# Performance work log

Measured on AMD Instinct MI355X. Metric: run time of the kernel, lower is better.

The kernel has to match this reference:

```python
import jax, jax.numpy as jnp
import numpy as np
from jax import lax

DIM = 512; HEADS = 8; HD = DIM // HEADS; SM = 16; NS = 3
B = 8; HH = 32; WW = 32; N = HH * WW; HL = DIM // 4


def setup_inputs() -> dict:
    key = jax.random.key(0)
    ks = iter(jax.random.split(key, 64))
    def g(shape, s=0.02):
        return jax.random.normal(next(ks), shape, dtype=jnp.float32) * s
    z = lambda *sh: jnp.zeros(sh, jnp.float32)
    inp = {
        'x': jax.random.normal(next(ks), (B, N, DIM), dtype=jnp.float32),
        'H': HH, 'W': WW,
        'qkv_w': g((NS, 3 * DIM, DIM)),
        'proj_w': g((DIM, DIM)), 'proj_b': z(DIM),
        'pos_sw': g((HEADS, SM, HD, 2)), 'neg_sw': g((HEADS, SM, HD, 2)),
        'spec_mix': jnp.ones((HEADS, SM), jnp.float32),
        'ca_w1': g((DIM // 2, DIM)), 'ca_b1': z(DIM // 2),
        'ca_w2': g((HEADS * 4, DIM // 2)), 'ca_b2': z(HEADS * 4),
        'lstm_wih_f': g((4 * HL, DIM)), 'lstm_whh_f': g((4 * HL, HL)),
        'lstm_bih_f': z(4 * HL), 'lstm_bhh_f': z(4 * HL),
        'lstm_wih_b': g((4 * HL, DIM)), 'lstm_whh_b': g((4 * HL, HL)),
        'lstm_bih_b': z(4 * HL), 'lstm_bhh_b': z(4 * HL),
        'mha_in_w': g((3 * DIM, DIM)), 'mha_in_b': z(3 * DIM),
        'mha_out_w': g((DIM, DIM)), 'mha_out_b': z(DIM),
        'ge_w1': g((DIM // 2, DIM)), 'ge_b1': z(DIM // 2),
        'ge_w2': g((HEADS * 2, DIM // 2)), 'ge_b2': z(HEADS * 2),
        'spw': jnp.ones((NS, HEADS, HD), jnp.float32),
        'dwc_w5': g((HD, 1, 5, 5), 0.05), 'dwc_b5': z(HD),
        'dwc_w7': g((HD, 1, 7, 7), 0.05), 'dwc_b7': z(HD),
        'dwc_w9': g((HD, 1, 9, 9), 0.05), 'dwc_b9': z(HD),
        'mode_w': jnp.ones((3,), jnp.float32) / 3.0,
    }
    return inp


def reference(x, H, W, qkv_w, proj_w, proj_b, pos_sw, neg_sw, spec_mix,
              ca_w1, ca_b1, ca_w2, ca_b2,
              lstm_wih_f, lstm_whh_f, lstm_bih_f, lstm_bhh_f,
              lstm_wih_b, lstm_whh_b, lstm_bih_b, lstm_bhh_b,
              mha_in_w, mha_in_b, mha_out_w, mha_out_b,
              ge_w1, ge_b1, ge_w2, ge_b2, spw,
              dwc_w5, dwc_b5, dwc_w7, dwc_b7, dwc_w9, dwc_b9, mode_w):
    Bn, Nn, C = x.shape
    heads = HEADS; hd = C // heads

    # ---------- DynamicContextEncoder ----------
    def lstm_dir(xs, wih, whh, bih, bhh):
        # xs: (N, B, C); PyTorch gate order i,f,g,o
        gates_x = xs @ wih.T + (bih + bhh)
        hdim = whh.shape[1]
        def step(carry, gx):
            h, c = carry
            gi = gx + h @ whh.T
            i, f, gg, o = jnp.split(gi, 4, axis=-1)
            c = jax.nn.sigmoid(f) * c + jax.nn.sigmoid(i) * jnp.tanh(gg)
            h = jax.nn.sigmoid(o) * jnp.tanh(c)
            return (h, c), h
        z0 = jnp.zeros((xs.shape[1], hdim), xs.dtype)
        _, hs = lax.scan(step, (z0, z0), gates_x)
        return hs

    xs = jnp.swapaxes(x, 0, 1)  # (N, B, C)
    h_f = lstm_dir(xs, lstm_wih_f, lstm_whh_f, lstm_bih_f, lstm_bhh_f)
    h_b = lstm_dir(xs[::-1], lstm_wih_b, lstm_whh_b, lstm_bih_b, lstm_bhh_b)[::-1]
    local_ctx = jnp.concatenate([h_f, h_b], -1).mean(0)  # (B, dim//2)
    local_ctx = jnp.pad(local_ctx, ((0, 0), (0, C - local_ctx.shape[1])))

    nh2 = heads // 2; hd2 = C // nh2
    qkv_c = x @ mha_in_w.T + mha_in_b
    qc, kc, vc = jnp.split(qkv_c, 3, -1)
    sh = lambda t: t.reshape(Bn, Nn, nh2, hd2).transpose(0, 2, 1, 3)
    qc, kc, vc = sh(qc), sh(kc), sh(vc)
    attn = jax.nn.softmax(jnp.einsum('bhnd,bhmd->bhnm', qc, kc) / float(np.sqrt(hd2)), -1)
    ac = jnp.einsum('bhnm,bhmd->bhnd', attn, vc).transpose(0, 2, 1, 3).reshape(Bn, Nn, C)
    ac = ac @ mha_out_w.T + mha_out_b
    combined = x.mean(1) + local_ctx + ac.mean(1)
    coeffs = jax.nn.sigmoid(jax.nn.relu(combined @ ca_w1.T + ca_b1) @ ca_w2.T + ca_b2)
    coeffs = coeffs.reshape(Bn, heads, 4)

    # ---------- GradientInformedMixer coefficients (x_grad is zeros) ----------
    gz = jnp.zeros((Bn, C), x.dtype)
    gmix = jax.nn.softmax((jnp.tanh(gz @ ge_w1.T + ge_b1) @ ge_w2.T + ge_b2).reshape(Bn, heads, 2), -1)

    # ---------- SpectralPolarityMixer ----------
    smix = jax.nn.softmax(spec_mix, -1).mean(-1)[None, :, None, None]  # per-head scalar
    wp = (pos_sw[..., 0] + 1j * pos_sw[..., 1])[:, :SM, :SM]
    wn = (neg_sw[..., 0] + 1j * neg_sw[..., 1])[:, :SM, :SM]

    def spectral(t):
        tf = jnp.fft.rfft2(t)[:, :, :SM, :SM]
        tp = jnp.fft.irfft2(tf * wp[None], s=(Nn, hd))
        tn = jnp.fft.irfft2(tf * wn[None], s=(Nn, hd))
        return tp + tn * smix

    def safe_pow(t, p):  # relu(t)**p with safe grads
        tp = jnp.where(t > 0, t, 1.0)
        return jnp.where(t > 0, tp ** p, 0.0)

    mw = jax.nn.softmax(mode_w, 0)
    def dwc(xi, w, b):
        return lax.conv_general_dilated(xi, w, (1, 1), 'SAME',
                                        feature_group_count=xi.shape[1],
                                        dimension_numbers=('NCHW', 'OIHW', 'NCHW')) + b[None, :, None, None]

    c0, c1, c2, c3 = [coeffs[:, :, i][:, :, None, None] for i in range(4)]
    g0, g1 = gmix[:, :, 0][:, :, None, None], gmix[:, :, 1][:, :, None, None]

    outs = []
    for s in range(NS):
        qkv = (x @ qkv_w[s].T).reshape(Bn, Nn, 3, heads, hd).transpose(2, 0, 3, 1, 4)
        q, k, v = qkv[0], qkv[1], qkv[2]  # (B, heads, N, hd)
        q = spectral(q); k = spectral(k)
        p = (1.0 + jnp.abs(spw[s]))[None, :, None, :]
        q_pos = safe_pow(q, p); q_neg = safe_pow(-q, p)
        k_pos = safe_pow(k, p); k_neg = safe_pow(-k, p)
        kvpp = jnp.einsum('bhnd,bhne->bhde', k_pos, v)
        kvnn = jnp.einsum('bhnd,bhne->bhde', k_neg, v)
        z = (jnp.einsum('bhnd,bhd->bhn', q_pos, k_pos.sum(2))
             + jnp.einsum('bhnd,bhd->bhn', q_neg, k_neg.sum(2)) + 1e-6)[..., None]
        same = (c0 * jnp.einsum('bhnd,bhde->bhne', q_pos, kvpp)
                + c1 * jnp.einsum('bhnd,bhde->bhne', q_neg, kvnn)) / z
        opp = (c2 * jnp.einsum('bhnd,bhde->bhne', q_pos, kvnn)
               + c3 * jnp.einsum('bhnd,bhde->bhne', q_neg, kvpp)) / z
        mixed = g0 * same + g1 * opp
        v_img = v.reshape(Bn * heads, H, W, hd).transpose(0, 3, 1, 2)
        vcv = mw[0] * dwc(v_img, dwc_w5, dwc_b5) + mw[1] * dwc(v_img, dwc_w7, dwc_b7) + mw[2] * dwc(v_img, dwc_w9, dwc_b9)
        vcv = vcv.transpose(0, 2, 3, 1).reshape(Bn, heads, Nn, hd)
        outs.append(mixed + vcv)

    out = jnp.stack(outs).mean(0).transpose(0, 2, 1, 3).reshape(Bn, Nn, C)
    return out @ proj_w.T + proj_b
```

## Files before the change

kernel.cpp:

```cpp
#include <hip/hip_runtime.h>
#include <hip/hip_bf16.h>
#include <math.h>

typedef __bf16 bf16x8 __attribute__((ext_vector_type(8)));
typedef __bf16 bf16x4 __attribute__((ext_vector_type(4)));
typedef float  f32x4  __attribute__((ext_vector_type(4)));

#define MFMA(a,b,c) __builtin_amdgcn_mfma_f32_16x16x32_bf16(a, b, c, 0, 0, 0)
#define LOG2E 1.4426950408889634f

static constexpr size_t OFF_R0    = 0;
static constexpr size_t OFF_GXT   = 12582912;
static constexpr size_t OFF_ACCUM = OFF_GXT;
static constexpr size_t OFF_FINAL = OFF_GXT + 4194304;
static constexpr size_t SOFF      = OFF_GXT + 8388608;
static constexpr size_t OFF_ROWSUM= SOFF;
static constexpr size_t OFF_ACMP  = OFF_ROWSUM;
static constexpr size_t OFF_COLW  = OFF_ROWSUM + 32768;
static constexpr size_t OFF_BM    = OFF_COLW;
static constexpr size_t OFF_ACM   = OFF_COLW + 524288;
static constexpr size_t OFF_XMEAN = OFF_ACM + 4096;
static constexpr size_t OFF_LC    = OFF_XMEAN + 4096;
static constexpr size_t OFF_COEF  = OFF_LC + 2048;
static constexpr size_t OFF_GMIX  = OFF_COEF + 256;
// ... 99 lines not shown
    if (dy>=-3 && dy<=3 && dx>=-3 && dx<=3) v += mw[1]*w7[d*49 + (dy+3)*7 + (dx+3)];
    if (dy>=-2 && dy<=2 && dx>=-2 && dx<=2) v += mw[0]*w5[d*25 + (dy+2)*5 + (dx+2)];
    ws[OFF_CONV9+f] = v;
  }
  if (tid<64) ws[OFF_CBIAS+tid] = mw[0]*b5[tid]+mw[1]*b7[tid]+mw[2]*b9[tid];
  for (int f=tid; f<2048; f+=256){
    int h=f>>8, k1=(f>>4)&15, k2=f&15;
    int src = ((h*16+k1)*64 + k2)*2;
    ws[OFF_WEFF+2*f]   = pos_sw[src]   + 0.0625f*neg_sw[src];
    ws[OFF_WEFF+2*f+1] = pos_sw[src+1] + 0.0625f*neg_sw[src+1];
  }
  for (int f=tid; f<1536; f+=256) ws[OFF_PPOW+f] = 1.0f + fabsf(spw[f]);
  for (int f=tid; f<1024; f+=256){
    int e=f>>4, k2=f&15; int ph=(e*k2)&63;
    float th = (float)ph * (6.283185307179586f/64.0f);
    ws[OFF_W2+2*f]   = cosf(th);
    ws[OFF_W2+2*f+1] = -sinf(th);
  }
  __bf16* w1cs = (__bf16*)(ws + OFF_W1CS);
  for (int f=tid; f<32768; f+=256){
    int r=f>>10, m=f&1023; int k1=r&15; int ph=(k1*m)&1023;
    float th = (float)ph * (6.283185307179586f/1024.0f);
    w1cs[f] = (__bf16)((r<16)?cosf(th):-sinf(th));
  }
  __bf16* w1t = (__bf16*)(ws + OFF_W1T);
  for (int f=tid; f<32768; f+=256){
    int n=f>>5, r=f&31; int k1=r&15; int ph=(k1*n)&1023;
    float th = (float)ph * (6.283185307179586f/1024.0f);
    w1t[f] = (__bf16)((r<16)?cosf(th):sinf(th));
  }
}


__device__ __forceinline__ void d_gemm(const __bf16* __restrict__ A, const __bf16* __restrict__ W,
                                       const float* __restrict__ bias, __bf16* __restrict__ C,
                                       int NB_N, int N, int K, int o, int nwg, int tid, char* smraw){
  __bf16 (*As)[40] = (__bf16(*)[40])smraw;
  __bf16 (*Ws)[40] = (__bf16(*)[40])(smraw + 10240);
  int cpx = nwg >> 3;
  int wg = (o & 7)*cpx + (o >> 3);
  int n0 = (wg % NB_N) * 128, m0 = (wg / NB_N) * 128;
  int l = tid & 63, wid = tid >> 6, lr = l & 15, lg = l >> 4;
  int wr = wid >> 1, wc = wid & 1;
  f32x4 acc[4][4];
  #pragma unroll
  for (int i=0;i<4;++i){ acc[i][0]=fz4(); acc[i][1]=fz4(); acc[i][2]=fz4(); acc[i][3]=fz4(); }
  int srow = tid >> 1, sk = (tid & 1) * 16;
  const __bf16* Ap = A + (size_t)(m0 + srow) * K + sk;
  const __bf16* Wp = W + (size_t)(n0 + srow) * K + sk;
  for (int k0 = 0; k0 < K; k0 += 32){
    bf16x8 a0 = *(const bf16x8*)(Ap), a1 = *(const bf16x8*)(Ap+8);
    bf16x8 w0 = *(const bf16x8*)(Wp), w1 = *(const bf16x8*)(Wp+8);
    Ap += 32; Wp += 32;
    __syncthreads();
    *(bf16x8*)&As[srow][sk]   = a0;  *(bf16x8*)&As[srow][sk+8] = a1;
    *(bf16x8*)&Ws[srow][sk]   = w0;  *(bf16x8*)&Ws[srow][sk+8] = w1;
    __syncthreads();
    bf16x8 aF[4], bF[4];
    #pragma unroll
    for (int mf=0;mf<4;++mf) aF[mf] = *(const bf16x8*)&As[wr*64+mf*16+lr][lg*8];
    #pragma unroll
    for (int nf=0;nf<4;++nf) bF[nf] = *(const bf16x8*)&Ws[wc*64+nf*16+lr][lg*8];
    #pragma unroll
    for (int mf=0;mf<4;++mf)
      #pragma unroll
      for (int nf=0;nf<4;++nf) acc[mf][nf] = MFMA(aF[mf], bF[nf], acc[mf][nf]);
  }
  #pragma unroll
  for (int mf=0;mf<4;++mf)
    #pragma unroll
    for (int nf=0;nf<4;++nf){
      int row = m0 + wr*64 + mf*16 + lg*4;
      int col = n0 + wc*64 + nf*16 + lr;
      float bv = bias ? bias[col] : 0.f;
      #pragma unroll
      for (int r=0;r<4;++r) C[(size_t)(row+r)*N + col] = (__bf16)(acc[mf][nf][r] + bv);
    }
}

template<int PHASE>
__device__ __forceinline__ void d_lstm(const float* __restrict__ whh_f, const float* __restrict__ whh_b,
                                       const __bf16* __restrict__ gates, float* __restrict__ lc,
                                       float* __restrict__ state, int bid, int tid, char* smraw){
  int dir = bid >> 3, b = bid & 7;
  const float* __restrict__ whh = dir ? whh_b : whh_f;
  const __bf16* gx = gates + (size_t)b*1048576;
  int w=tid>>6, l=tid&63, lr=l&15, lg=l>>4;
  bf16x8 wf[4][2][4];
  #pragma unroll
  for (int q=0;q<4;++q)
    #pragma unroll
    for (int t=0;t<2;++t)
      #pragma unroll
      for (int kc=0;kc<4;++kc){
        const float* p = whh + (size_t)(q*128 + w*32 + t*16 + lr)*128 + kc*32 + lg*8;
        bf16x8 v;
        #pragma unroll
        for (int j=0;j<8;++j) v[j]=(__bf16)p[j];
        wf[q][t][kc]=v;
      }
  __bf16 (*hbuf)[132] = (__bf16(*)[132])smraw;
  int tsel = l&1, rsel = (l>>1)&3;
  int hrow = w*32 + tsel*16 + lg*4 + rsel;
  float* st = state + bid*768 + tid*3;
  float cs, hs;
  if (PHASE==0){
    for (int i=tid; i<264; i+=256) ((__bf16*)hbuf)[i] = (__bf16)0.0f;
    cs=0.f; hs=0.f;
  } else {
    cs = st[0]; hs = st[1];
    hbuf[0][hrow] = (__bf16)st[2];
  }
  long t0 = (PHASE==0) ? (dir?1023:0) : (dir?511:512);
  long tstride = dir ? -1024 : 1024;
  long toff = t0*1024 + dir*512 + hrow;
  float g0[4], g1[4], g2[4], g3[4];
  #pragma unroll
  for (int q=0;q<4;++q) g0[q] = (float)gx[toff + q*128];
  toff += tstride;
  #pragma unroll
  for (int q=0;q<4;++q) g1[q] = (float)gx[toff + q*128];
  toff += tstride;
  #pragma unroll
  for (int q=0;q<4;++q) g2[q] = (float)gx[toff + q*128];
  toff += tstride;
  #pragma unroll
  for (int q=0;q<4;++q) g3[q] = (float)gx[toff + q*128];
  toff += tstride;
  __syncthreads();

#define LSTM_STEP(RB, WB, G) { \
    float gq[4]; \
    _Pragma("unroll") for (int q=0;q<4;++q) gq[q]=G[q]; \
    _Pragma("unroll") for (int q=0;q<4;++q) G[q] = (float)gx[toff + q*128]; \
    toff += tstride; \
    if (toff < 0) toff = 0; \
    if (toff > 1048000) toff = 1048000; \
    bf16x8 hf[4]; \
    _Pragma("unroll") for (int kc=0;kc<4;++kc) hf[kc] = *(const bf16x8*)&hbuf[RB][kc*32 + lg*8]; \
    f32x4 acc[4][2]; \
    _Pragma("unroll") for (int q=0;q<4;++q){ acc[q][0]=fz4(); acc[q][1]=fz4(); } \
    _Pragma("unroll") for (int kc=0;kc<4;++kc) \
      _Pragma("unroll") for (int q=0;q<4;++q){ \
        acc[q][0] = MFMA(wf[q][0][kc], hf[kc], acc[q][0]); \
        acc[q][1] = MFMA(wf[q][1][kc], hf[kc], acc[q][1]); } \
    float gv[4]; \
    _Pragma("unroll") for (int q=0;q<4;++q){ \
      f32x4 v0 = acc[q][0], v1 = acc[q][1]; \
      float a01 = (rsel&1) ? v0[1] : v0[0]; \
      float a23 = (rsel&1) ? v0[3] : v0[2]; \
      float av  = (rsel&2) ? a23 : a01; \
      float b01 = (rsel&1) ? v1[1] : v1[0]; \
      float b23 = (rsel&1) ? v1[3] : v1[2]; \
      float bv  = (rsel&2) ? b23 : b01; \
      gv[q] = (tsel ? bv : av) + gq[q]; } \
    float ii=sigm(gv[0]), ff=sigm(gv[1]), gg=tanhx(gv[2]), oo=sigm(gv[3]); \
    cs = ff*cs + ii*gg; \
    float hv = oo*tanhx(cs); \
    hs += hv; \
    if (!(l&8)) hbuf[WB][hrow] = (__bf16)hv; \
    asm volatile("s_waitcnt lgkmcnt(0)" ::: "memory"); \
    __builtin_amdgcn_sched_barrier(0); \
    __builtin_amdgcn_s_barrier(); \
    __builtin_amdgcn_sched_barrier(0); }

  for (int it=0; it<128; ++it){
    LSTM_STEP(0, 1, g0)
    LSTM_STEP(1, 0, g1)
    LSTM_STEP(0, 1, g2)
    LSTM_STEP(1, 0, g3)
  }
#undef LSTM_STEP
  if (PHASE==0){
    st[0]=cs; st[1]=hs; st[2]=(float)hbuf[0][hrow];
  } else {
    if (!(l&8)) lc[b*256 + dir*128 + hrow] = hs*(1.f/1024.f);
  }
}

__device__ __forceinline__ void d_xmean(const float* __restrict__ x, float* __restrict__ xpart,
                                        int f, int tid){
  int sl = f & 15, b = f >> 4;
  #pragma unroll
  for (int cc=0; cc<2; ++cc){
    int c = tid + cc*256;
    float s=0.f;
    for (int n=sl*64; n<sl*64+64; ++n) s += x[((size_t)(b*1024+n))*512 + c];
    xpart[((size_t)(b*16+sl))*512 + c] = s;
  }
}

template<int MODE>
__device__ __forceinline__ void d_mha(const __bf16* __restrict__ qkv, float* __restrict__ rowsum,
                                      float* __restrict__ colw, int f, int tid, char* smraw){
  int rb = f & 3, h2 = (f>>2) & 3, b = f >> 4;
  __bf16 (*Qs)[136] = (__bf16(*)[136])smraw;
  __bf16 (*Ks)[136] = (__bf16(*)[136])(smraw + 69632);
  int l=tid&63, w=tid>>6, lr=l&15, lg=l>>4;
  {
    const float qs = LOG2E / sqrtf(128.0f);
    int row = tid;
    const __bf16* p = qkv + ((size_t)(b*1024 + rb*256 + row))*1536 + h2*128;
    #pragma unroll
    for (int cc=0; cc<128; cc+=8){
      bf16x8 u = *(const bf16x8*)(p+cc);
      bf16x8 v;
      #pragma unroll
      for (int j=0;j<8;++j) v[j]=(__bf16)((float)u[j]*qs);
      *(bf16x8*)&Qs[row][cc] = v;
    }
  }
  float rs[4][4];
  if (MODE==1){
    #pragma unroll
    for (int mf=0;mf<4;++mf){ rs[mf][0]=0.f; rs[mf][1]=0.f; rs[mf][2]=0.f; rs[mf][3]=0.f; }
  } else {
    #pragma unroll
    for (int mf=0;mf<4;++mf)
      #pragma unroll
      for (int r=0;r<4;++r)
        rs[mf][r] = 1.0f / rowsum[((size_t)(b*4+h2))*1024 + rb*256 + w*64 + mf*16 + lg*4 + r];
  }
  for (int mc=0; mc<8; ++mc){
    __syncthreads();
    {
      int row = tid>>1, co = (tid&1)*64;
      const __bf16* p = qkv + ((size_t)(b*1024 + mc*128 + row))*1536 + 512 + h2*128 + co;
      #pragma unroll
      for (int cc=0; cc<64; cc+=8)
        *(bf16x8*)&Ks[row][co+cc] = *(const bf16x8*)(p+cc);
    }
    __syncthreads();
    f32x4 acc[4][8];
    #pragma unroll
    for (int mf=0;mf<4;++mf)
      #pragma unroll
      for (int nf=0;nf<8;++nf) acc[mf][nf]=fz4();
    #pragma unroll
    for (int ks=0;ks<4;++ks){
      bf16x8 aF[4], bFv[8];
      #pragma unroll
      for (int mf=0;mf<4;++mf) aF[mf] = *(const bf16x8*)&Qs[w*64+mf*16+lr][ks*32+lg*8];
      #pragma unroll
      for (int nf=0;nf<8;++nf) bFv[nf] = *(const bf16x8*)&Ks[nf*16+lr][ks*32+lg*8];
      #pragma unroll
      for (int mf=0;mf<4;++mf)
        #pragma unroll
        for (int nf=0;nf<8;++nf) acc[mf][nf] = MFMA(aF[mf], bFv[nf], acc[mf][nf]);
    }
    if (MODE==1){
      #pragma unroll
      for (int mf=0;mf<4;++mf)
        #pragma unroll
        for (int nf=0;nf<8;++nf)
          #pragma unroll
          for (int r=0;r<4;++r) rs[mf][r] += exp2f(acc[mf][nf][r]);
    } else {
      #pragma unroll
      for (int nf=0;nf<8;++nf){
        float cv = 0.f;
// ... 96 lines not shown
      hbl[d*32 + 16 + k1] = (__bf16)(-hi*inv);
    }
  }
  __syncthreads();
  const __bf16* w1t = (const __bf16*)(ws + OFF_W1T);
  bf16x8 bF[4];
  #pragma unroll
  for (int nf=0;nf<4;++nf) bF[nf] = *(const bf16x8*)&hbl[(nf*16+lr)*32 + lg*8];
  for (int pass=0; pass<4; ++pass){
    int rowbase = w*256 + pass*64;
    f32x4 acc[4][4];
    #pragma unroll
    for (int mf=0;mf<4;++mf){ acc[mf][0]=fz4(); acc[mf][1]=fz4(); acc[mf][2]=fz4(); acc[mf][3]=fz4(); }
    #pragma unroll
    for (int mf=0;mf<4;++mf){
      bf16x8 aF = *(const bf16x8*)(w1t + (size_t)(rowbase+mf*16+lr)*32 + lg*8);
      #pragma unroll
      for (int nf=0;nf<4;++nf) acc[mf][nf] = MFMA(aF, bF[nf], acc[mf][nf]);
    }
    #pragma unroll
    for (int mf=0;mf<4;++mf)
      #pragma unroll
      for (int nf=0;nf<4;++nf)
        #pragma unroll
        for (int r=0;r<4;++r){
          int n = rowbase + mf*16 + lg*4 + r;
          int d = nf*16 + lr;
          qkv[((size_t)(b*1024+n))*1536 + colbase + d] = (__bf16)acc[mf][nf][r];
        }
  }
}

__device__ __forceinline__ void d_conv(const __bf16* __restrict__ qkv, const float* __restrict__ ws,
                                       float* __restrict__ accum, int f, int tid, char* smraw, bool init){
  int sl = f & 3, h = (f>>2)&7, b = f>>5;
  float (*vs)[16] = (float(*)[16])smraw;
  float (*wc)[81] = (float(*)[81])(smraw + 65536);
  float* cb       = (float*)(smraw + 65536 + 5184);
  #pragma unroll
  for (int it=0; it<8; ++it){
    int flat = tid + 256*it;
    int pix = flat>>1, cg = (flat&1)*8;
    bf16x8 u = *(const bf16x8*)(qkv + ((size_t)(b*1024+pix))*1536 + 1024 + h*64 + sl*16 + cg);
    #pragma unroll
    for (int j=0;j<8;++j) vs[pix][cg+j] = (float)u[j];
  }
  for (int f2=tid; f2<16*81; f2+=256) wc[f2/81][f2%81] = ws[OFF_CONV9 + (size_t)(sl*16 + f2/81)*81 + (f2%81)];
  if (tid<16) cb[tid] = ws[OFF_CBIAS + sl*16 + tid];
  __syncthreads();
  #pragma unroll
  for (int cc=0; cc<2; ++cc){
    int col = tid + 256*cc;
    int c = col & 15, x = col >> 4;
    float a[32];
    #pragma unroll
    for (int y=0;y<32;++y) a[y]=0.f;
    #pragma unroll
    for (int dx=-4; dx<=4; ++dx){
      int xx = x+dx;
      bool xv = (xx>=0)&&(xx<32);
      float colv[40];
      #pragma unroll
      for (int i=0;i<40;++i){
        int yy = i-4;
        colv[i] = (xv && yy>=0 && yy<32) ? vs[yy*32+xx][c] : 0.f;
      }
      #pragma unroll
      for (int dy=0; dy<9; ++dy){
        float wv = wc[c][dy*9 + dx+4];
        #pragma unroll
        for (int y=0;y<32;++y) a[y] += wv*colv[y+dy];
      }
    }
    float bias = cb[c];
    #pragma unroll
    for (int y=0;y<32;++y){
      size_t oi = ((size_t)((b*8+h)*1024) + y*32 + x)*64 + sl*16 + c;
      if (init) accum[oi] = a[y] + bias;
      else      accum[oi] += a[y] + bias;
    }
  }
}


__global__ __launch_bounds__(256,2) void k_gemm_bf(const __bf16* __restrict__ A, const __bf16* __restrict__ W,
                                                   const float* __restrict__ bias, __bf16* __restrict__ C,
                                                   int NB_N, int N, int K){
  __shared__ __align__(16) char sm[20480];
  d_gemm(A, W, bias, C, NB_N, N, K, blockIdx.x, gridDim.x, threadIdx.x, sm);
}

__global__ __launch_bounds__(256,1) void k_mega1(const float* __restrict__ whh_f, const float* __restrict__ whh_b,
                                                 const __bf16* __restrict__ gates, float* __restrict__ ws,
                                                 const float* __restrict__ x,
                                                 const __bf16* __restrict__ xb, const __bf16* __restrict__ mwb,
                                                 const __bf16* __restrict__ qwb,
                                                 const float* __restrict__ mha_in_b,
                                                 __bf16* __restrict__ qkvA, __bf16* __restrict__ qkvB){
  __shared__ __align__(16) char sm[20480];
  int bid = blockIdx.x, tid = threadIdx.x;
  if (bid < 16)         d_lstm<0>(whh_f, whh_b, gates, ws+OFF_LC, ws+OFF_STATE, bid, tid, sm);
  else if (bid < 784)   d_gemm(xb, mwb, mha_in_b, qkvA, 12, 1536, 512, bid-16, 768, tid, sm);
  else if (bid < 1552)  d_gemm(xb, qwb, nullptr,   qkvB, 12, 1536, 512, bid-784, 768, tid, sm);
  else                  d_xmean(x, ws+OFF_XP2, bid-1552, tid);
}

__global__ __launch_bounds__(256,1) void k_mega2(const float* __restrict__ whh_f, const float* __restrict__ whh_b,
                                                 const __bf16* __restrict__ gates, float* __restrict__ ws,
                                                 const __bf16* __restrict__ qkvA, __bf16* __restrict__ qkvB,
                                                 float* __restrict__ accum){
  __shared__ __align__(16) char sm[104448];
  int bid = blockIdx.x, tid = threadIdx.x;
  if (bid < 16)        d_lstm<1>(whh_f, whh_b, gates, ws+OFF_LC, ws+OFF_STATE, bid, tid, sm);
  else if (bid < 144)  d_spec(qkvB, ws, bid-16, tid, sm);
  else if (bid < 272)  d_mha<1>(qkvA, ws+OFF_ROWSUM, ws+OFF_COLW, bid-144, tid, sm);
  else                 d_conv(qkvB, ws, accum, bid-272, tid, sm, true);
}

__global__ __launch_bounds__(256,2) void k_specconv(__bf16* __restrict__ qkv, const float* __restrict__ ws,
                                                    float* __restrict__ accum){
  __shared__ __align__(16) char sm[80896];
  int bid = blockIdx.x, tid = threadIdx.x;
  if (bid < 128) d_spec(qkv, ws, bid, tid, sm);
  else           d_conv(qkv, ws, accum, bid-128, tid, sm, false);
}

__global__ __launch_bounds__(256,1) void k_mha2_w(const __bf16* __restrict__ qkv, float* __restrict__ rowsum,
                                                  float* __restrict__ colw){
  __shared__ __align__(16) char sm[104448];
  d_mha<2>(qkv, rowsum, colw, blockIdx.x, threadIdx.x, sm);
}

__global__ void k_mha3(const __bf16* __restrict__ qkv, const float* __restrict__ colw, float* __restrict__ acmp){
  int h2 = blockIdx.x, b = blockIdx.y, ms = blockIdx.z;
  int tid = threadIdx.x;
  __shared__ float cwred[128];
  if (tid < 128){
    float cw=0.f;
    #pragma unroll
    for (int t16=0;t16<16;++t16) cw += colw[(((size_t)t16*8 + b)*4 + h2)*1024 + ms*128 + tid];
    cwred[tid]=cw;
  }
  __syncthreads();
  int e = tid & 127, half = tid >> 7;
  float s = 0.f;
  for (int ml = half*64; ml < half*64+64; ++ml)
    s += cwred[ml] * (float)qkv[((size_t)(b*1024 + ms*128 + ml))*1536 + 1024 + h2*128 + e];
  __shared__ float red[256];
  red[tid]=s; __syncthreads();
  if (tid<128) acmp[((size_t)(ms*8+b))*512 + h2*128 + e] = red[tid]+red[tid+128];
}

__global__ __launch_bounds__(256) void k_coeffs(float* __restrict__ ws,
                        const float* __restrict__ mow, const float* __restrict__ mob,
                        const float* __restrict__ ca_w1, const float* __restrict__ ca_b1,
                        const float* __restrict__ ca_w2, const float* __restrict__ ca_b2){
  int b = blockIdx.x, tid = threadIdx.x;
  __shared__ float av[512], comb[512], hid[256];
  for (int i=tid;i<512;i+=256){
    float s = 0.f;
    #pragma unroll
    for (int ms=0; ms<8; ++ms) s += ws[OFF_ACMP + ((size_t)(ms*8+b))*512 + i];
    av[i] = s*(1.f/1024.f);
  }
  __syncthreads();
  for (int c=tid;c<512;c+=256){
    float s = mob[c];
    for (int k=0;k<512;++k) s += mow[(size_t)c*512+k]*av[k];
    float xm = 0.f;
    #pragma unroll
    for (int sl=0; sl<16; ++sl) xm += ws[OFF_XP2 + ((size_t)(b*16+sl))*512 + c];
    comb[c] = s + xm*(1.f/1024.f) + ((c<256) ? ws[OFF_LC + b*256 + c] : 0.f);
  }
  __syncthreads();
  for (int j=tid;j<256;j+=256){
    float s = ca_b1[j];
    for (int k=0;k<512;++k) s += ca_w1[(size_t)j*512+k]*comb[k];
    hid[j] = fmaxf(s,0.f);
  }
  __syncthreads();
  if (tid<32){
    float s = ca_b2[tid];
    for (int k=0;k<256;++k) s += ca_w2[tid*256+k]*hid[k];
    ws[OFF_COEF + b*32 + tid] = 1.f/(1.f+expf(-s));
  }
}

__global__ __launch_bounds__(256,2) void k_polar_kv(const __bf16* __restrict__ qkv, float* __restrict__ ws,
                                                    int s){
  int h = blockIdx.x, b = blockIdx.y;
  int tid=threadIdx.x, l=tid&63, w=tid>>6, lr=l&15, lg=l>>4;
  __shared__ float plds[14300];
  __bf16* kpT = (__bf16*)plds;
  __bf16* knT = (__bf16*)((char*)plds + 17408);
  __bf16* vT  = (__bf16*)((char*)plds + 34816);
  float* scal = (float*)((char*)plds + 56576);
  float* pvs  = scal + 8;
  if (tid<4)  scal[tid] = ws[OFF_COEF + b*32 + h*4 + tid];
  if (tid==4) scal[4] = ws[OFF_GMIX + 2*h];
  if (tid==5) scal[5] = ws[OFF_GMIX + 2*h+1];
  if (tid<64) pvs[tid] = ws[OFF_PPOW + ((size_t)s*8+h)*64 + tid];
  for (int i=tid; i<16*136; i+=256) vT[64*136 + i] = (__bf16)((i<136)?1.0f:0.0f);
  f32x4 acc[4][5];
  #pragma unroll
  for (int mf=0;mf<4;++mf)
    #pragma unroll
    for (int nf=0;nf<5;++nf) acc[mf][nf]=fz4();
  for (int mc=0;mc<8;++mc){
    __syncthreads();
    #pragma unroll
    for (int it=0; it<16; ++it){
      int flat = tid + 256*it;
      int d = flat & 63, np = flat >> 6;
      int n = mc*128 + 2*np;
      const __bf16* kr = qkv + ((size_t)(b*1024+n))*1536 + 512 + h*64 + d;
      const __bf16* vr = qkv + ((size_t)(b*1024+n))*1536 + 1024 + h*64 + d;
      float p = pvs[d];
      float k0=(float)kr[0], k1=(float)kr[1536];
      float kp0,kn0,kp1,kn1;
      powpair(k0,p,kp0,kn0); powpair(k1,p,kp1,kn1);
      *(unsigned*)&kpT[d*136 + 2*np] = pk2(kp0,kp1);
      *(unsigned*)&knT[d*136 + 2*np] = pk2(kn0,kn1);
      *(unsigned*)&vT [d*136 + 2*np] = pk2b(vr[0], vr[1536]);
    }
    __syncthreads();
    const __bf16* A = (w&2)?knT:kpT;
    int kh = (w&1)*64;
    #pragma unroll
    for (int ks=0;ks<2;++ks){
      bf16x8 aF[4];
      #pragma unroll
      for (int mf=0;mf<4;++mf) aF[mf] = *(const bf16x8*)&A[(mf*16+lr)*136 + kh + ks*32 + lg*8];
      #pragma unroll
      for (int nf=0;nf<5;++nf){
        bf16x8 bFv = *(const bf16x8*)&vT[(nf*16+lr)*136 + kh + ks*32 + lg*8];
        #pragma unroll
        for (int mf=0;mf<4;++mf) acc[mf][nf] = MFMA(aF[mf], bFv, acc[mf][nf]);
      }
    }
  }
  __syncthreads();
  float* kvf = plds;
  if ((w&1)==0){
    int mat = w>>1;
    #pragma unroll
    for (int mf=0;mf<4;++mf)
      #pragma unroll
      for (int nf=0;nf<5;++nf)
        #pragma unroll
        for (int r=0;r<4;++r)
          kvf[((size_t)mat*64 + mf*16+lg*4+r)*80 + nf*16+lr] = acc[mf][nf][r];
  }
  __syncthreads();
  if (w&1){
    int mat = w>>1;
    #pragma unroll
    for (int mf=0;mf<4;++mf)
      #pragma unroll
      for (int nf=0;nf<5;++nf)
        #pragma unroll
        for (int r=0;r<4;++r)
          kvf[((size_t)mat*64 + mf*16+lg*4+r)*80 + nf*16+lr] += acc[mf][nf][r];
  }
  __syncthreads();
  __bf16* bmg = (__bf16*)(ws + OFF_BM) + (size_t)(b*8+h)*10240;
  {
    float c0=scal[0], c1=scal[1], c2=scal[2], c3=scal[3], g0=scal[4], g1=scal[5];
    for (int f=tid; f<80*128; f+=256){
      int e=f>>7, kk=f&127;
      float v;
      if (e<64){
        if (kk<64) v = g0*c0*kvf[kk*80+e] + g1*c2*kvf[(64+kk)*80+e];
        else { int k2=kk-64; v = g0*c1*kvf[(64+k2)*80+e] + g1*c3*kvf[k2*80+e]; }
      } else if (e==64){
        v = (kk<64) ? kvf[kk*80+64] : kvf[(64+(kk-64))*80+64];
      } else v = 0.f;
      bmg[f] = (__bf16)v;
    }
  }
}

__global__ __launch_bounds__(256,2) void k_polar_ap(const __bf16* __restrict__ qkv, const float* __restrict__ ws,
                                                    float* __restrict__ accum, int s){
  int pass8 = blockIdx.x, h = blockIdx.y, b = blockIdx.z;
  int tid=threadIdx.x, l=tid&63, w=tid>>6, lr=l&15, lg=l>>4;
  __shared__ __bf16 At[128*136];
  __shared__ __bf16 BmL[80*136];
  __shared__ float zb[128];
  __shared__ float pvs[64];
  if (tid<64) pvs[tid] = ws[OFF_PPOW + ((size_t)s*8+h)*64 + tid];
  {
    const __bf16* bmg = (const __bf16*)(ws + OFF_BM) + (size_t)(b*8+h)*10240;
    for (int u=tid; u<80*16; u+=256){
      int e=u>>4, kx=(u&15)*8;
      *(bf16x8*)&BmL[e*136+kx] = *(const bf16x8*)(bmg + e*128 + kx);
    }
  }
  __syncthreads();
  #pragma unroll
  for (int it=0; it<8; ++it){
    int flat = tid + 256*it;
    int row = flat>>4, dg = flat&15;
    int n = pass8*128 + row;
    const __bf16* qr = qkv + ((size_t)(b*1024+n))*1536 + h*64 + dg*4;
    bf16x4 u = *(const bf16x4*)qr;
    float qp[4], qn[4];
    #pragma unroll
    for (int j=0;j<4;++j) powpair((float)u[j], pvs[dg*4+j], qp[j], qn[j]);
    *(unsigned*)&At[row*136 + dg*4]        = pk2(qp[0],qp[1]);
    *(unsigned*)&At[row*136 + dg*4+2]      = pk2(qp[2],qp[3]);
    *(unsigned*)&At[row*136 + 64 + dg*4]   = pk2(qn[0],qn[1]);
    *(unsigned*)&At[row*136 + 64 + dg*4+2] = pk2(qn[2],qn[3]);
  }
  __syncthreads();
  f32x4 a2[2][5];
  #pragma unroll
  for (int mf=0;mf<2;++mf)
    #pragma unroll
    for (int nf=0;nf<5;++nf) a2[mf][nf]=fz4();
  #pragma unroll
  for (int ks=0;ks<4;++ks){
    bf16x8 aF[2];
    #pragma unroll
    for (int mf=0;mf<2;++mf) aF[mf] = *(const bf16x8*)&At[(w*32+mf*16+lr)*136 + ks*32 + lg*8];
    #pragma unroll
    for (int nf=0;nf<5;++nf){
      bf16x8 bFv = *(const bf16x8*)&BmL[(nf*16+lr)*136 + ks*32 + lg*8];
      #pragma unroll
      for (int mf=0;mf<2;++mf) a2[mf][nf] = MFMA(aF[mf], bFv, a2[mf][nf]);
    }
  }
  if (lr==0){
    #pragma unroll
    for (int mf=0;mf<2;++mf)
      #pragma unroll
      for (int r=0;r<4;++r) zb[w*32 + mf*16 + lg*4 + r] = a2[mf][4][r] + 1e-6f;
  }
  __syncthreads();
  #pragma unroll
  for (int mf=0;mf<2;++mf){
    float rz[4];
    #pragma unroll
    for (int r=0;r<4;++r) rz[r] = 1.0f / zb[w*32 + mf*16 + lg*4 + r];
    #pragma unroll
    for (int nf=0;nf<4;++nf)
      #pragma unroll
      for (int r=0;r<4;++r){
        int n = pass8*128 + w*32 + mf*16 + lg*4 + r;
        int e = nf*16 + lr;
        size_t oi = ((size_t)((b*8+h)*1024) + n)*64 + e;
        accum[oi] += a2[mf][nf][r]*rz[r];
      }
  }
}

__global__ __launch_bounds__(256,2) void k_gemm_acc(const float* __restrict__ accum, const __bf16* __restrict__ W,
                                                    const float* __restrict__ bias, float* __restrict__ C){
  const int N = 512, K = 512, NB_N = 4;
  __shared__ __bf16 As[128][40];
  __shared__ __bf16 Ws[128][40];
  int tid = threadIdx.x;
  int nwg = gridDim.x, o = blockIdx.x;
  int cpx = nwg >> 3;
  int wg = (o & 7)*cpx + (o >> 3);
  int n0 = (wg % NB_N) * 128, m0 = (wg / NB_N) * 128;
  int l = tid & 63, wid = tid >> 6, lr = l & 15, lg = l >> 4;
  int wr = wid >> 1, wc = wid & 1;
  f32x4 acc[4][4];
  #pragma unroll
  for (int i=0;i<4;++i){ acc[i][0]=fz4(); acc[i][1]=fz4(); acc[i][2]=fz4(); acc[i][3]=fz4(); }
  int srow = tid >> 1, sk = (tid & 1) * 16;
  int row = m0 + srow;
  int bb = row >> 10, nn = row & 1023;
  const float* Abase = accum + ((size_t)bb*8192 + nn)*64;
  const __bf16* Wp = W + (size_t)(n0 + srow) * K + sk;
  const float s3 = 1.0f/3.0f;
  for (int k0 = 0; k0 < K; k0 += 32){
    int c0 = k0 + sk;
    const float* Ap = Abase + (size_t)(c0>>6)*65536 + (c0&63);
    f32x4 a0=*(const f32x4*)(Ap), a1=*(const f32x4*)(Ap+4), a2=*(const f32x4*)(Ap+8), a3=*(const f32x4*)(Ap+12);
    bf16x8 w0 = *(const bf16x8*)(Wp), w1 = *(const bf16x8*)(Wp+8);
    Wp += 32;
    __syncthreads();
    bf16x8 va, vb;
    #pragma unroll
    for (int j=0;j<4;++j){ va[j]=(__bf16)(a0[j]*s3); va[j+4]=(__bf16)(a1[j]*s3);
                           vb[j]=(__bf16)(a2[j]*s3); vb[j+4]=(__bf16)(a3[j]*s3); }
    *(bf16x8*)&As[srow][sk]   = va;  *(bf16x8*)&As[srow][sk+8] = vb;
    *(bf16x8*)&Ws[srow][sk]   = w0;  *(bf16x8*)&Ws[srow][sk+8] = w1;
    __syncthreads();
    bf16x8 aF[4], bF[4];
    #pragma unroll
    for (int mf=0;mf<4;++mf) aF[mf] = *(const bf16x8*)&As[wr*64+mf*16+lr][lg*8];
    #pragma unroll
    for (int nf=0;nf<4;++nf) bF[nf] = *(const bf16x8*)&Ws[wc*64+nf*16+lr][lg*8];
    #pragma unroll
    for (int mf=0;mf<4;++mf)
      #pragma unroll
      for (int nf=0;nf<4;++nf) acc[mf][nf] = MFMA(aF[mf], bF[nf], acc[mf][nf]);
  }
  #pragma unroll
  for (int mf=0;mf<4;++mf)
    #pragma unroll
    for (int nf=0;nf<4;++nf){
      int orow = m0 + wr*64 + mf*16 + lg*4;
      int col = n0 + wc*64 + nf*16 + lr;
      float bv = bias[col];
      #pragma unroll
      for (int r=0;r<4;++r) C[(size_t)(orow+r)*N + col] = acc[mf][nf][r] + bv;
    }
}

extern "C" void kernel_launch(void* const* d_in, const int* in_sizes, int n_in,
                              void* d_out, int out_size, void* d_ws, size_t ws_size,
                              hipStream_t stream){
  const float* x        = (const float*)d_in[0];
  const float* qkv_w    = (const float*)d_in[3];
  const float* proj_w   = (const float*)d_in[4];
  const float* proj_b   = (const float*)d_in[5];
  const float* pos_sw   = (const float*)d_in[6];
  const float* neg_sw   = (const float*)d_in[7];
  const float* ca_w1    = (const float*)d_in[9];
  const float* ca_b1    = (const float*)d_in[10];
  const float* ca_w2    = (const float*)d_in[11];
  const float* ca_b2    = (const float*)d_in[12];
  const float* wih_f    = (const float*)d_in[13];
  const float* whh_f    = (const float*)d_in[14];
  const float* bih_f    = (const float*)d_in[15];
  const float* bhh_f    = (const float*)d_in[16];
  const float* wih_b    = (const float*)d_in[17];
  const float* whh_b    = (const float*)d_in[18];
  const float* bih_b    = (const float*)d_in[19];
  const float* bhh_b    = (const float*)d_in[20];
  const float* mha_in_w = (const float*)d_in[21];
  const float* mha_in_b = (const float*)d_in[22];
  const float* mha_out_w= (const float*)d_in[23];
  const float* mha_out_b= (const float*)d_in[24];
  const float* ge_b1    = (const float*)d_in[26];
  const float* ge_w2    = (const float*)d_in[27];
  const float* ge_b2    = (const float*)d_in[28];
  const float* spw      = (const float*)d_in[29];
  const float* w5 = (const float*)d_in[30]; const float* b5 = (const float*)d_in[31];
  const float* w7 = (const float*)d_in[32]; const float* b7 = (const float*)d_in[33];
  const float* w9 = (const float*)d_in[34]; const float* b9 = (const float*)d_in[35];
  const float* mode_w = (const float*)d_in[36];
  float* ws  = (float*)d_ws;
  float* out = (float*)d_out;
  __bf16* xb     = (__bf16*)(ws + OFF_XB);
  __bf16* qwb    = (__bf16*)(ws + OFF_QW);
  __bf16* mwb    = (__bf16*)(ws + OFF_MW2);
  __bf16* wfb    = (__bf16*)(ws + OFF_WFB);
  __bf16* pwb    = (__bf16*)(ws + OFF_PWB);
  __bf16* qkvA   = (__bf16*)(ws + OFF_R0);
  __bf16* qkvB   = qkvA + 12582912;
  __bf16* gatesb = (__bf16*)out;

  k_const<<<1,256,0,stream>>>(ge_b1, ge_w2, ge_b2, mode_w, w5,b5,w7,b7,w9,b9,
                              pos_sw, neg_sw, spw, bih_f,bhh_f,bih_b,bhh_b, ws);
  k_cvt_all<<<3968,256,0,stream>>>(x, qkv_w, mha_in_w, wih_f, wih_b, proj_w, ws);
  k_gemm_bf<<<512,256,0,stream>>>(xb, wfb, ws+OFF_LBIAS, gatesb, 8, 1024, 512);
  k_mega1<<<1680,256,0,stream>>>(whh_f, whh_b, gatesb, ws, x, xb, mwb, qwb, mha_in_b, qkvA, qkvB);
  k_mega2<<<528,256,0,stream>>>(whh_f, whh_b, gatesb, ws, qkvA, qkvB, ws+OFF_ACCUM);
  k_mha2_w<<<128,256,0,stream>>>(qkvA, ws+OFF_ROWSUM, ws+OFF_COLW);
  k_mha3<<<dim3(4,8,8),256,0,stream>>>(qkvA, ws+OFF_COLW, ws+OFF_ACMP);
  k_coeffs<<<8,256,0,stream>>>(ws, mha_out_w, mha_out_b, ca_w1, ca_b1, ca_w2, ca_b2);
  k_polar_kv<<<dim3(8,8),256,0,stream>>>(qkvB, ws, 0);
  k_polar_ap<<<dim3(8,8,8),256,0,stream>>>(qkvB, ws, ws+OFF_ACCUM, 0);
  for (int s=1; s<3; ++s){
    k_gemm_bf<<<768,256,0,stream>>>(xb, qwb + (size_t)s*786432, nullptr, qkvB, 12, 1536, 512);
    k_specconv<<<384,256,0,stream>>>(qkvB, ws, ws+OFF_ACCUM);
    k_polar_kv<<<dim3(8,8),256,0,stream>>>(qkvB, ws, s);
    k_polar_ap<<<dim3(8,8,8),256,0,stream>>>(qkvB, ws, ws+OFF_ACCUM, s);
  }
  k_gemm_acc<<<256,256,0,stream>>>(ws+OFF_ACCUM, pwb, proj_b, out);
}
```

Measured before the change: 1.337 ms.

## Software-pipeline spectral scales by fusing polar, conv and next-scale QKV GEMM kernels

Turns the polar KV and apply kernels into device functions and builds mixed mega-kernels. Each one runs the polar attention for scale s in the same launch as the QKV GEMM, spectral transform or depthwise conv for scale s+1, using ping-pong qkvA/qkvB buffers. This cuts the number of launches and fills idle CUs during the small polar kernels. It also sets a higher wave priority for the LSTM recurrence blocks inside the mega-kernels. In exchange the schedule is more complex, the buffer reuse is fragile, and the shared-memory footprint rises.

```diff
diff --git a/kernel.cpp b/kernel.cpp
--- a/kernel.cpp
+++ b/kernel.cpp
@@ -205,6 +205,7 @@
 __device__ __forceinline__ void d_lstm(const float* __restrict__ whh_f, const float* __restrict__ whh_b,
                                        const __bf16* __restrict__ gates, float* __restrict__ lc,
                                        float* __restrict__ state, int bid, int tid, char* smraw){
+  __builtin_amdgcn_s_setprio(1);
   int dir = bid >> 3, b = bid & 7;
   const float* __restrict__ whh = dir ? whh_b : whh_f;
   const __bf16* gx = gates + (size_t)b*1048576;
@@ -299,6 +300,7 @@
   } else {
     if (!(l&8)) lc[b*256 + dir*128 + hrow] = hs*(1.f/1024.f);
   }
+  __builtin_amdgcn_s_setprio(0);
 }
 
 __device__ __forceinline__ void d_xmean(const float* __restrict__ x, float* __restrict__ xpart,
@@ -561,6 +563,174 @@
   }
 }
 
+__device__ __forceinline__ void d_polar_kv(const __bf16* __restrict__ qkv, float* __restrict__ ws,
+                                           int s, int f, int tid, char* smraw){
+  int h = f & 7, b = f >> 3;
+  int l=tid&63, w=tid>>6, lr=l&15, lg=l>>4;
+  float* plds = (float*)smraw;
+  __bf16* kpT = (__bf16*)smraw;
+  __bf16* knT = (__bf16*)(smraw + 17408);
+  __bf16* vT  = (__bf16*)(smraw + 34816);
+  float* scal = (float*)(smraw + 56576);
+  float* pvs  = scal + 8;
+  if (tid<4)  scal[tid] = ws[OFF_COEF + b*32 + h*4 + tid];
+  if (tid==4) scal[4] = ws[OFF_GMIX + 2*h];
+  if (tid==5) scal[5] = ws[OFF_GMIX + 2*h+1];
+  if (tid<64) pvs[tid] = ws[OFF_PPOW + ((size_t)s*8+h)*64 + tid];
+  for (int i=tid; i<16*136; i+=256) vT[64*136 + i] = (__bf16)((i<136)?1.0f:0.0f);
+  f32x4 acc[4][5];
+  #pragma unroll
+  for (int mf=0;mf<4;++mf)
+    #pragma unroll
+    for (int nf=0;nf<5;++nf) acc[mf][nf]=fz4();
+  for (int mc=0;mc<8;++mc){
+    __syncthreads();
+    #pragma unroll
+    for (int it=0; it<16; ++it){
+      int flat = tid + 256*it;
+      int d = flat & 63, np = flat >> 6;
+      int n = mc*128 + 2*np;
+      const __bf16* kr = qkv + ((size_t)(b*1024+n))*1536 + 512 + h*64 + d;
+      const __bf16* vr = qkv + ((size_t)(b*1024+n))*1536 + 1024 + h*64 + d;
+      float p = pvs[d];
+      float k0=(float)kr[0], k1=(float)kr[1536];
+      float kp0,kn0,kp1,kn1;
+      powpair(k0,p,kp0,kn0); powpair(k1,p,kp1,kn1);
+      *(unsigned*)&kpT[d*136 + 2*np] = pk2(kp0,kp1);
+      *(unsigned*)&knT[d*136 + 2*np] = pk2(kn0,kn1);
+      *(unsigned*)&vT [d*136 + 2*np] = pk2b(vr[0], vr[1536]);
+    }
+    __syncthreads();
+    const __bf16* A = (w&2)?knT:kpT;
+    int kh = (w&1)*64;
+    #pragma unroll
+    for (int ks=0;ks<2;++ks){
+      bf16x8 aF[4];
+      #pragma unroll
+      for (int mf=0;mf<4;++mf) aF[mf] = *(const bf16x8*)&A[(mf*16+lr)*136 + kh + ks*32 + lg*8];
+      #pragma unroll
+      for (int nf=0;nf<5;++nf){
+        bf16x8 bFv = *(const bf16x8*)&vT[(nf*16+lr)*136 + kh + ks*32 + lg*8];
+        #pragma unroll
+        for (int mf=0;mf<4;++mf) acc[mf][nf] = MFMA(aF[mf], bFv, acc[mf][nf]);
+      }
+    }
+  }
+  __syncthreads();
+  float* kvf = plds;
+  if ((w&1)==0){
+    int mat = w>>1;
+    #pragma unroll
+    for (int mf=0;mf<4;++mf)
+      #pragma unroll
+      for (int nf=0;nf<5;++nf)
+        #pragma unroll
+        for (int r=0;r<4;++r)
+          kvf[((size_t)mat*64 + mf*16+lg*4+r)*80 + nf*16+lr] = acc[mf][nf][r];
+  }
+  __syncthreads();
+  if (w&1){
+    int mat = w>>1;
+    #pragma unroll
+    for (int mf=0;mf<4;++mf)
+      #pragma unroll
+      for (int nf=0;nf<5;++nf)
+        #pragma unroll
+        for (int r=0;r<4;++r)
+          kvf[((size_t)mat*64 + mf*16+lg*4+r)*80 + nf*16+lr] += acc[mf][nf][r];
+  }
+  __syncthreads();
+  __bf16* bmg = (__bf16*)(ws + OFF_BM) + (size_t)(b*8+h)*10240;
+  {
+    float c0=scal[0], c1=scal[1], c2=scal[2], c3=scal[3], g0=scal[4], g1=scal[5];
+    for (int f2=tid; f2<80*128; f2+=256){
+      int e=f2>>7, kk=f2&127;
+      float v;
+      if (e<64){
+        if (kk<64) v = g0*c0*kvf[kk*80+e] + g1*c2*kvf[(64+kk)*80+e];
+        else { int k2=kk-64; v = g0*c1*kvf[(64+k2)*80+e] + g1*c3*kvf[k2*80+e]; }
+      } else if (e==64){
+        v = (kk<64) ? kvf[kk*80+64] : kvf[(64+(kk-64))*80+64];
+      } else v = 0.f;
+      bmg[f2] = (__bf16)v;
+    }
+  }
+}
+
+__device__ __forceinline__ void d_polar_ap(const __bf16* __restrict__ qkv, const float* __restrict__ ws,
+                                           float* __restrict__ accum, int s, int f, int tid, char* smraw){
+  int pass8 = f & 7, h = (f>>3)&7, b = f>>6;
+  int l=tid&63, w=tid>>6, lr=l&15, lg=l>>4;
+  __bf16* At  = (__bf16*)smraw;
+  __bf16* BmL = (__bf16*)(smraw + 34816);
+  float* zb   = (float*)(smraw + 56576);
+  float* pvs  = (float*)(smraw + 57088);
+  if (tid<64) pvs[tid] = ws[OFF_PPOW + ((size_t)s*8+h)*64 + tid];
+  {
+    const __bf16* bmg = (const __bf16*)(ws + OFF_BM) + (size_t)(b*8+h)*10240;
+    for (int u=tid; u<80*16; u+=256){
+      int e=u>>4, kx=(u&15)*8;
+      *(bf16x8*)&BmL[e*136+kx] = *(const bf16x8*)(bmg + e*128 + kx);
+    }
+  }
+  __syncthreads();
+  #pragma unroll
+  for (int it=0; it<8; ++it){
+    int flat = tid + 256*it;
+    int row = flat>>4, dg = flat&15;
+    int n = pass8*128 + row;
+    const __bf16* qr = qkv + ((size_t)(b*1024+n))*1536 + h*64 + dg*4;
+    bf16x4 u = *(const bf16x4*)qr;
+    float qp[4], qn[4];
+    #pragma unroll
+    for (int j=0;j<4;++j) powpair((float)u[j], pvs[dg*4+j], qp[j], qn[j]);
+    *(unsigned*)&At[(row*136) + dg*4]        = pk2(qp[0],qp[1]);
+    *(unsigned*)&At[(row*136) + dg*4+2]      = pk2(qp[2],qp[3]);
+    *(unsigned*)&At[(row*136) + 64 + dg*4]   = pk2(qn[0],qn[1]);
+    *(unsigned*)&At[(row*136) + 64 + dg*4+2] = pk2(qn[2],qn[3]);
+  }
+  __syncthreads();
+  f32x4 a2[2][5];
+  #pragma unroll
+  for (int mf=0;mf<2;++mf)
+    #pragma unroll
+    for (int nf=0;nf<5;++nf) a2[mf][nf]=fz4();
+  #pragma unroll
+  for (int ks=0;ks<4;++ks){
+    bf16x8 aF[2];
+    #pragma unroll
+    for (int mf=0;mf<2;++mf) aF[mf] = *(const bf16x8*)&At[(w*32+mf*16+lr)*136 + ks*32 + lg*8];
+    #pragma unroll
+    for (int nf=0;nf<5;++nf){
+      bf16x8 bFv = *(const bf16x8*)&BmL[(nf*16+lr)*136 + ks*32 + lg*8];
+      #pragma unroll
+      for (int mf=0;mf<2;++mf) a2[mf][nf] = MFMA(aF[mf], bFv, a2[mf][nf]);
+    }
+  }
+  if (lr==0){
+    #pragma unroll
+    for (int mf=0;mf<2;++mf)
+      #pragma unroll
+      for (int r=0;r<4;++r) zb[w*32 + mf*16 + lg*4 + r] = a2[mf][4][r] + 1e-6f;
+  }
+  __syncthreads();
+  #pragma unroll
+  for (int mf=0;mf<2;++mf){
+    float rz[4];
+    #pragma unroll
+    for (int r=0;r<4;++r) rz[r] = 1.0f / zb[w*32 + mf*16 + lg*4 + r];
+    #pragma unroll
+    for (int nf=0;nf<4;++nf)
+      #pragma unroll
+      for (int r=0;r<4;++r){
+        int n = pass8*128 + w*32 + mf*16 + lg*4 + r;
+        int e = nf*16 + lr;
+        size_t oi = ((size_t)((b*8+h)*1024) + n)*64 + e;
+        accum[oi] += a2[mf][nf][r]*rz[r];
+      }
+  }
+}
+
 
 __global__ __launch_bounds__(256,2) void k_gemm_bf(const __bf16* __restrict__ A, const __bf16* __restrict__ W,
                                                    const float* __restrict__ bias, __bf16* __restrict__ C,
@@ -596,12 +766,47 @@
   else                 d_conv(qkvB, ws, accum, bid-272, tid, sm, true);
 }
 
-__global__ __launch_bounds__(256,2) void k_specconv(__bf16* __restrict__ qkv, const float* __restrict__ ws,
-                                                    float* __restrict__ accum){
+__global__ __launch_bounds__(256,2) void k_mA(const __bf16* __restrict__ qr, float* __restrict__ ws, int s,
+                                              const __bf16* __restrict__ xb, const __bf16* __restrict__ Wg,
+                                              __bf16* __restrict__ qw){
+  __shared__ __align__(16) char sm[57344];
+  int bid = blockIdx.x, tid = threadIdx.x;
+  if (bid < 64) d_polar_kv(qr, ws, s, bid, tid, sm);
+  else          d_gemm(xb, Wg, nullptr, qw, 12, 1536, 512, bid-64, 768, tid, sm);
+}
+
+__global__ __launch_bounds__(256,2) void k_mB(const __bf16* __restrict__ qr, float* __restrict__ ws,
+                                              float* __restrict__ accum, int s,
+                                              __bf16* __restrict__ qs2){
   __shared__ __align__(16) char sm[80896];
   int bid = blockIdx.x, tid = threadIdx.x;
-  if (bid < 128) d_spec(qkv, ws, bid, tid, sm);
-  else           d_conv(qkv, ws, accum, bid-128, tid, sm, false);
+  if (bid < 512) d_polar_ap(qr, ws, accum, s, bid, tid, sm);
+  else           d_spec(qs2, ws, bid-512, tid, sm);
+}
+
+__global__ __launch_bounds__(256,2) void k_mC(const __bf16* __restrict__ qc, float* __restrict__ ws,
+                                              float* __restrict__ accum, int s,
+                                              const __bf16* __restrict__ xb, const __bf16* __restrict__ Wg,
+                                              __bf16* __restrict__ qw){
+  __shared__ __align__(16) char sm[70784];
+  int bid = blockIdx.x, tid = threadIdx.x;
+  if (bid < 256)      d_conv(qc, ws, accum, bid, tid, sm, false);
+  else if (bid < 320) d_polar_kv(qc, ws, s, bid-256, tid, sm);
+  else                d_gemm(xb, Wg, nullptr, qw, 12, 1536, 512, bid-320, 768, tid, sm);
+}
+
+__global__ __launch_bounds__(256,2) void k_mE(const __bf16* __restrict__ qc, float* __restrict__ ws,
+                                              float* __restrict__ accum, int s){
+  __shared__ __align__(16) char sm[70784];
+  int bid = blockIdx.x, tid = threadIdx.x;
+  if (bid < 256) d_conv(qc, ws, accum, bid, tid, sm, false);
+  else           d_polar_kv(qc, ws, s, bid-256, tid, sm);
+}
+
+__global__ __launch_bounds__(256,2) void k_mF(const __bf16* __restrict__ qr, float* __restrict__ ws,
+                                              float* __restrict__ accum, int s){
+  __shared__ __align__(16) char sm[57600];
+  d_polar_ap(qr, ws, accum, s, blockIdx.x, threadIdx.x, sm);
 }
 
 __global__ __launch_bounds__(256,1) void k_mha2_w(const __bf16* __restrict__ qkv, float* __restrict__ rowsum,
@@ -662,174 +867,6 @@
     float s = ca_b2[tid];
     for (int k=0;k<256;++k) s += ca_w2[tid*256+k]*hid[k];
     ws[OFF_COEF + b*32 + tid] = 1.f/(1.f+expf(-s));
-  }
-}
-
-__global__ __launch_bounds__(256,2) void k_polar_kv(const __bf16* __restrict__ qkv, float* __restrict__ ws,
-                                                    int s){
-  int h = blockIdx.x, b = blockIdx.y;
-  int tid=threadIdx.x, l=tid&63, w=tid>>6, lr=l&15, lg=l>>4;
-  __shared__ float plds[14300];
-  __bf16* kpT = (__bf16*)plds;
-  __bf16* knT = (__bf16*)((char*)plds + 17408);
-  __bf16* vT  = (__bf16*)((char*)plds + 34816);
-  float* scal = (float*)((char*)plds + 56576);
-  float* pvs  = scal + 8;
-  if (tid<4)  scal[tid] = ws[OFF_COEF + b*32 + h*4 + tid];
-  if (tid==4) scal[4] = ws[OFF_GMIX + 2*h];
-  if (tid==5) scal[5] = ws[OFF_GMIX + 2*h+1];
-  if (tid<64) pvs[tid] = ws[OFF_PPOW + ((size_t)s*8+h)*64 + tid];
-  for (int i=tid; i<16*136; i+=256) vT[64*136 + i] = (__bf16)((i<136)?1.0f:0.0f);
-  f32x4 acc[4][5];
-  #pragma unroll
-  for (int mf=0;mf<4;++mf)
-    #pragma unroll
-    for (int nf=0;nf<5;++nf) acc[mf][nf]=fz4();
-  for (int mc=0;mc<8;++mc){
-    __syncthreads();
-    #pragma unroll
-    for (int it=0; it<16; ++it){
-      int flat = tid + 256*it;
-      int d = flat & 63, np = flat >> 6;
-      int n = mc*128 + 2*np;
-      const __bf16* kr = qkv + ((size_t)(b*1024+n))*1536 + 512 + h*64 + d;
-      const __bf16* vr = qkv + ((size_t)(b*1024+n))*1536 + 1024 + h*64 + d;
-      float p = pvs[d];
-      float k0=(float)kr[0], k1=(float)kr[1536];
-      float kp0,kn0,kp1,kn1;
-      powpair(k0,p,kp0,kn0); powpair(k1,p,kp1,kn1);
-      *(unsigned*)&kpT[d*136 + 2*np] = pk2(kp0,kp1);
-      *(unsigned*)&knT[d*136 + 2*np] = pk2(kn0,kn1);
-      *(unsigned*)&vT [d*136 + 2*np] = pk2b(vr[0], vr[1536]);
-    }
-    __syncthreads();
-    const __bf16* A = (w&2)?knT:kpT;
-    int kh = (w&1)*64;
-    #pragma unroll
-    for (int ks=0;ks<2;++ks){
-      bf16x8 aF[4];
-      #pragma unroll
-      for (int mf=0;mf<4;++mf) aF[mf] = *(const bf16x8*)&A[(mf*16+lr)*136 + kh + ks*32 + lg*8];
-      #pragma unroll
-      for (int nf=0;nf<5;++nf){
-        bf16x8 bFv = *(const bf16x8*)&vT[(nf*16+lr)*136 + kh + ks*32 + lg*8];
-        #pragma unroll
-        for (int mf=0;mf<4;++mf) acc[mf][nf] = MFMA(aF[mf], bFv, acc[mf][nf]);
-      }
-    }
-  }
-  __syncthreads();
-  float* kvf = plds;
-  if ((w&1)==0){
-    int mat = w>>1;
-    #pragma unroll
-    for (int mf=0;mf<4;++mf)
-      #pragma unroll
-      for (int nf=0;nf<5;++nf)
-        #pragma unroll
-        for (int r=0;r<4;++r)
-          kvf[((size_t)mat*64 + mf*16+lg*4+r)*80 + nf*16+lr] = acc[mf][nf][r];
-  }
-  __syncthreads();
-  if (w&1){
-    int mat = w>>1;
-    #pragma unroll
-    for (int mf=0;mf<4;++mf)
-      #pragma unroll
-      for (int nf=0;nf<5;++nf)
-        #pragma unroll
-        for (int r=0;r<4;++r)
-          kvf[((size_t)mat*64 + mf*16+lg*4+r)*80 + nf*16+lr] += acc[mf][nf][r];
-  }
-  __syncthreads();
-  __bf16* bmg = (__bf16*)(ws + OFF_BM) + (size_t)(b*8+h)*10240;
-  {
-    float c0=scal[0], c1=scal[1], c2=scal[2], c3=scal[3], g0=scal[4], g1=scal[5];
-    for (int f=tid; f<80*128; f+=256){
-      int e=f>>7, kk=f&127;
-      float v;
-      if (e<64){
-        if (kk<64) v = g0*c0*kvf[kk*80+e] + g1*c2*kvf[(64+kk)*80+e];
-        else { int k2=kk-64; v = g0*c1*kvf[(64+k2)*80+e] + g1*c3*kvf[k2*80+e]; }
-      } else if (e==64){
-        v = (kk<64) ? kvf[kk*80+64] : kvf[(64+(kk-64))*80+64];
-      } else v = 0.f;
-      bmg[f] = (__bf16)v;
-    }
-  }
-}
-
-__global__ __launch_bounds__(256,2) void k_polar_ap(const __bf16* __restrict__ qkv, const float* __restrict__ ws,
-                                                    float* __restrict__ accum, int s){
-  int pass8 = blockIdx.x, h = blockIdx.y, b = blockIdx.z;
-  int tid=threadIdx.x, l=tid&63, w=tid>>6, lr=l&15, lg=l>>4;
-  __shared__ __bf16 At[128*136];
-  __shared__ __bf16 BmL[80*136];
-  __shared__ float zb[128];
-  __shared__ float pvs[64];
-  if (tid<64) pvs[tid] = ws[OFF_PPOW + ((size_t)s*8+h)*64 + tid];
-  {
-    const __bf16* bmg = (const __bf16*)(ws + OFF_BM) + (size_t)(b*8+h)*10240;
-    for (int u=tid; u<80*16; u+=256){
-      int e=u>>4, kx=(u&15)*8;
-      *(bf16x8*)&BmL[e*136+kx] = *(const bf16x8*)(bmg + e*128 + kx);
-    }
-  }
-  __syncthreads();
-  #pragma unroll
-  for (int it=0; it<8; ++it){
-    int flat = tid + 256*it;
-    int row = flat>>4, dg = flat&15;
-    int n = pass8*128 + row;
-    const __bf16* qr = qkv + ((size_t)(b*1024+n))*1536 + h*64 + dg*4;
-    bf16x4 u = *(const bf16x4*)qr;
-    float qp[4], qn[4];
-    #pragma unroll
-    for (int j=0;j<4;++j) powpair((float)u[j], pvs[dg*4+j], qp[j], qn[j]);
-    *(unsigned*)&At[row*136 + dg*4]        = pk2(qp[0],qp[1]);
-    *(unsigned*)&At[row*136 + dg*4+2]      = pk2(qp[2],qp[3]);
-    *(unsigned*)&At[row*136 + 64 + dg*4]   = pk2(qn[0],qn[1]);
-    *(unsigned*)&At[row*136 + 64 + dg*4+2] = pk2(qn[2],qn[3]);
-  }
-  __syncthreads();
-  f32x4 a2[2][5];
-  #pragma unroll
-  for (int mf=0;mf<2;++mf)
-    #pragma unroll
-    for (int nf=0;nf<5;++nf) a2[mf][nf]=fz4();
-  #pragma unroll
-  for (int ks=0;ks<4;++ks){
-    bf16x8 aF[2];
-    #pragma unroll
-    for (int mf=0;mf<2;++mf) aF[mf] = *(const bf16x8*)&At[(w*32+mf*16+lr)*136 + ks*32 + lg*8];
-    #pragma unroll
-    for (int nf=0;nf<5;++nf){
-      bf16x8 bFv = *(const bf16x8*)&BmL[(nf*16+lr)*136 + ks*32 + lg*8];
-      #pragma unroll
-      for (int mf=0;mf<2;++mf) a2[mf][nf] = MFMA(aF[mf], bFv, a2[mf][nf]);
-    }
-  }
-  if (lr==0){
-    #pragma unroll
-    for (int mf=0;mf<2;++mf)
-      #pragma unroll
-      for (int r=0;r<4;++r) zb[w*32 + mf*16 + lg*4 + r] = a2[mf][4][r] + 1e-6f;
-  }
-  __syncthreads();
-  #pragma unroll
-  for (int mf=0;mf<2;++mf){
-    float rz[4];
-    #pragma unroll
-    for (int r=0;r<4;++r) rz[r] = 1.0f / zb[w*32 + mf*16 + lg*4 + r];
-    #pragma unroll
-    for (int nf=0;nf<4;++nf)
-      #pragma unroll
-      for (int r=0;r<4;++r){
-        int n = pass8*128 + w*32 + mf*16 + lg*4 + r;
-        int e = nf*16 + lr;
-        size_t oi = ((size_t)((b*8+h)*1024) + n)*64 + e;
-        accum[oi] += a2[mf][nf][r]*rz[r];
-      }
   }
 }
 
@@ -943,13 +980,11 @@
   k_mha2_w<<<128,256,0,stream>>>(qkvA, ws+OFF_ROWSUM, ws+OFF_COLW);
   k_mha3<<<dim3(4,8,8),256,0,stream>>>(qkvA, ws+OFF_COLW, ws+OFF_ACMP);
   k_coeffs<<<8,256,0,stream>>>(ws, mha_out_w, mha_out_b, ca_w1, ca_b1, ca_w2, ca_b2);
-  k_polar_kv<<<dim3(8,8),256,0,stream>>>(qkvB, ws, 0);
-  k_polar_ap<<<dim3(8,8,8),256,0,stream>>>(qkvB, ws, ws+OFF_ACCUM, 0);
-  for (int s=1; s<3; ++s){
-    k_gemm_bf<<<768,256,0,stream>>>(xb, qwb + (size_t)s*786432, nullptr, qkvB, 12, 1536, 512);
-    k_specconv<<<384,256,0,stream>>>(qkvB, ws, ws+OFF_ACCUM);
-    k_polar_kv<<<dim3(8,8),256,0,stream>>>(qkvB, ws, s);
-    k_polar_ap<<<dim3(8,8,8),256,0,stream>>>(qkvB, ws, ws+OFF_ACCUM, s);
-  }
+  k_mA<<<832,256,0,stream>>>(qkvB, ws, 0, xb, qwb + 786432, qkvA);
+  k_mB<<<640,256,0,stream>>>(qkvB, ws, ws+OFF_ACCUM, 0, qkvA);
+  k_mC<<<1088,256,0,stream>>>(qkvA, ws, ws+OFF_ACCUM, 1, xb, qwb + 2*786432, qkvB);
+  k_mB<<<640,256,0,stream>>>(qkvA, ws, ws+OFF_ACCUM, 1, qkvB);
+  k_mE<<<320,256,0,stream>>>(qkvB, ws, ws+OFF_ACCUM, 2);
+  k_mF<<<512,256,0,stream>>>(qkvB, ws, ws+OFF_ACCUM, 2);
   k_gemm_acc<<<256,256,0,stream>>>(ws+OFF_ACCUM, pwb, proj_b, out);
 }
```

Measured after the change: 1.281 ms (median of 3 runs). 1.04x faster.
